# Optimization experiments

Hardware: AMD Instinct MI355X
Metric: run time of the kernel (lower is better)

The kernel has to match this reference:

```python
import jax, jax.numpy as jnp
import numpy as np

EPS = 1e-5
DIM_HEAD = 64
HEADS = 8

def layernorm(x, gamma, beta):
    mu = jnp.mean(x, axis=-1, keepdims=True)
    var = jnp.var(x, axis=-1, keepdims=True)
    return (x - mu) * jax.lax.rsqrt(var + EPS) * gamma + beta

def setup_inputs() -> dict:
    key = jax.random.key(0)
    ks = jax.random.split(key, 8)
    b, n, dh = 1, 896, 3072       # batch, enformer seq len, enformer_hidden_dim
    c, j, dc = 64, 127, 1024      # num contexts (tracks), context len, context_dim
    inner = HEADS * DIM_HEAD      # 512
    return {
        "embeddings": jax.random.normal(ks[0], (b, n, dh), jnp.float32),
        "context": jax.random.normal(ks[1], (c, j, dc), jnp.float32),
        "context_mask": jax.random.randint(ks[2], (b, j), 0, 2) > 0,
        "q_gamma": jnp.ones((dh,), jnp.float32),
        "q_beta": jnp.zeros((dh,), jnp.float32),
        "kv_gamma": jnp.ones((dc,), jnp.float32),
        "kv_beta": jnp.zeros((dc,), jnp.float32),
        "Wq": jax.random.normal(ks[3], (dh, inner), jnp.float32) * 0.02,
        "Wkv": jax.random.normal(ks[4], (dc, 2 * inner), jnp.float32) * 0.02,
        "null_k": jax.random.normal(ks[5], (inner,), jnp.float32),
        "null_v": jax.random.normal(ks[6], (inner,), jnp.float32),
        "Wo": jax.random.normal(ks[7], (inner, dh), jnp.float32) * 0.02,
        "bo": jnp.zeros((dh,), jnp.float32),
        "Wp": jax.random.normal(jax.random.fold_in(key, 9), (dh, 1), jnp.float32) * 0.02,
        "bp": jnp.zeros((1,), jnp.float32),
    }

def reference(embeddings, context, context_mask, q_gamma, q_beta, kv_gamma, kv_beta,
              Wq, Wkv, null_k, null_v, Wo, bo, Wp, bp):
    h, d = HEADS, DIM_HEAD
    scale = d ** -0.5
    b, n, dh = embeddings.shape
    c = context.shape[0]
    # projections
    q = layernorm(embeddings, q_gamma, q_beta) @ Wq            # (b, n, h*d)
    kv = layernorm(context, kv_gamma, kv_beta) @ Wkv           # (c, j, 2*h*d)
    k, v = jnp.split(kv, 2, axis=-1)
    # prepend null key/value token
    k = jnp.concatenate([jnp.broadcast_to(null_k, (c, 1, h * d)), k], axis=1)
    v = jnp.concatenate([jnp.broadcast_to(null_v, (c, 1, h * d)), v], axis=1)
    # split heads: (b, h, i, d) / (c, h, j, d)
    q = q.reshape(b, n, h, d).transpose(0, 2, 1, 3)
    k = k.reshape(c, -1, h, d).transpose(0, 2, 1, 3)
    v = v.reshape(c, -1, h, d).transpose(0, 2, 1, 3)
    sim = jnp.einsum('bhid,chjd->bchij', q, k) * scale         # (b, c, h, i, j+1)
    # mask: pad with True for the null token, broadcast over c, h, i
    mask = jnp.pad(context_mask, ((0, 0), (1, 0)), constant_values=True)
    sim = jnp.where(mask[:, None, None, None, :], sim, -jnp.finfo(sim.dtype).max)
    attn = jax.nn.softmax(sim, axis=-1)
    out = jnp.einsum('bchij,chjd->bchid', attn, v)             # (b, c, h, i, d)
    out = out.transpose(0, 1, 3, 2, 4).reshape(b, c, n, h * d)  # (b, c, n, h*d)
    branch = out @ Wo + bo                                     # (b, c, n, dh)
    emb = embeddings[:, None] + branch                         # (b, c, n, dh)
    pred = jax.nn.softplus((emb @ Wp + bp)[..., 0])            # (b, c, n)
    return pred.transpose(0, 2, 1)                             # (b, n, c)
```

## Files before the change

kernel.cpp:

```cpp
#include <hip/hip_runtime.h>
#include <math.h>

#define N_SEQ   896
#define DH      3072
#define NCTX    64
#define JLEN    127
#define DC      1024
#define HEADS   8
#define DHEAD   64
#define INNER   512
#define MKV     8128
#define MKVPAD  8192

typedef __bf16 bf16x8 __attribute__((ext_vector_type(8)));
typedef float  f32x4  __attribute__((ext_vector_type(4)));

#define OFF_EDOT   0LL
#define OFF_QBF    (OFF_EDOT + N_SEQ)
#define OFF_KBF    (OFF_QBF  + (long long)N_SEQ*INNER/2)
#define OFF_VPM    (OFF_KBF  + (long long)NCTX*128*INNER/2)
#define OFF_VPNULL (OFF_VPM  + (long long)MKV*8)
#define OFF_WOP    (OFF_VPNULL + 8)
#define OFF_BOP    (OFF_WOP  + INNER)
#define OFF_SBUF   (OFF_BOP  + 16)
#define OFF_ANQ    (OFF_SBUF + (long long)NCTX*HEADS*N_SEQ)
#define OFF_ANKV   (OFF_ANQ  + (long long)N_SEQ*DH/2)
#define OFF_WQT    (OFF_ANKV + (long long)MKVPAD*DC/2)
#define OFF_WKT    (OFF_WQT  + (long long)INNER*DH/2)
#define OFF_WVPT   (OFF_WKT  + (long long)INNER*DC/2)
#define OFF_QSL    (OFF_WVPT + 16*1024/2)

__device__ __forceinline__ void async_copy16(const __bf16* g, __bf16* l) {
    __builtin_amdgcn_global_load_lds(
        (const __attribute__((address_space(1))) unsigned int*)g,
        (__attribute__((address_space(3))) unsigned int*)l,
        16, 0, 0);
}

template <int P>
__device__ __forceinline__
void ln_row(const float* __restrict__ x,
            const float* __restrict__ gamma, const float* __restrict__ beta,
            const float* __restrict__ wp,
            __bf16* __restrict__ o, float* __restrict__ dotout) {
    const int K = P * 1024;
    float4 xv[P];
    float s = 0.f, ss = 0.f, dp = 0.f;
    #pragma unroll
    for (int p = 0; p < P; ++p) {
        xv[p] = *(const float4*)&x[p * 1024 + threadIdx.x * 4];
        s  += xv[p].x + xv[p].y + xv[p].z + xv[p].w;
        ss += xv[p].x * xv[p].x + xv[p].y * xv[p].y
            + xv[p].z * xv[p].z + xv[p].w * xv[p].w;
        if (wp) {
            float4 w4 = *(const float4*)&wp[p * 1024 + threadIdx.x * 4];
            dp += xv[p].x * w4.x + xv[p].y * w4.y + xv[p].z * w4.z + xv[p].w * w4.w;
        }
    }
    #pragma unroll
    for (int ofs = 32; ofs > 0; ofs >>= 1) {
        s  += __shfl_down(s,  ofs);
        ss += __shfl_down(ss, ofs);
        dp += __shfl_down(dp, ofs);
    }
    __shared__ float red[3][4];
    __shared__ float sh_mu, sh_rstd;
    int lane = threadIdx.x & 63, w = threadIdx.x >> 6;
    if (lane == 0) { red[0][w] = s; red[1][w] = ss; red[2][w] = dp; }
    __syncthreads();
    if (threadIdx.x == 0) {
        float S  = red[0][0] + red[0][1] + red[0][2] + red[0][3];
        float SS = red[1][0] + red[1][1] + red[1][2] + red[1][3];
        float m = S / K;
        sh_mu = m;
        sh_rstd = rsqrtf(SS / K - m * m + 1e-5f);
        if (dotout) *dotout = red[2][0] + red[2][1] + red[2][2] + red[2][3];
    }
    __syncthreads();
    float m = sh_mu, r = sh_rstd;
    #pragma unroll
    for (int p = 0; p < P; ++p) {
        int col = p * 1024 + threadIdx.x * 4;
        float4 g4 = *(const float4*)&gamma[col];
        float4 b4 = *(const float4*)&beta[col];
        __bf16 ov[4];
        ov[0] = (__bf16)((xv[p].x - m) * r * g4.x + b4.x);
        ov[1] = (__bf16)((xv[p].y - m) * r * g4.y + b4.y);
        ov[2] = (__bf16)((xv[p].z - m) * r * g4.z + b4.z);
        ov[3] = (__bf16)((xv[p].w - m) * r * g4.w + b4.w);
        *(ushort4*)&o[col] = *(ushort4*)ov;
    }
}

__global__ __launch_bounds__(256)
void ln_wop_kernel(const float* __restrict__ emb, const float* __restrict__ ctx,
                   const float* __restrict__ qg, const float* __restrict__ qb,
                   const float* __restrict__ kvg, const float* __restrict__ kvb,
                   const float* __restrict__ Wp, const float* __restrict__ Wo,
                   const float* __restrict__ bo,
                   __bf16* __restrict__ anq, __bf16* __restrict__ ankv,
                   float* __restrict__ edot, float* __restrict__ wop,
                   float* __restrict__ bop) {
    int b = blockIdx.x;
    if (b < N_SEQ) {
        ln_row<3>(emb + (long long)b * DH, qg, qb, Wp,
                  anq + (long long)b * DH, edot + b);
    } else if (b < N_SEQ + MKV) {
        int r = b - N_SEQ;
        ln_row<1>(ctx + (long long)r * DC, kvg, kvb, nullptr,
                  ankv + (long long)r * DC, nullptr);
    } else {
        int r = b - (N_SEQ + MKV);
        const float* src = (r < INNER) ? (Wo + (long long)r * DH) : bo;
        float s = 0.f;
        for (int k = threadIdx.x; k < DH; k += 256) s += src[k] * Wp[k];
        #pragma unroll
        for (int o = 32; o > 0; o >>= 1) s += __shfl_down(s, o);
        __shared__ float red2[4];
        int lane = threadIdx.x & 63, w = threadIdx.x >> 6;
        if (lane == 0) red2[w] = s;
        __syncthreads();
        if (threadIdx.x == 0) {
            float S = red2[0] + red2[1] + red2[2] + red2[3];
            if (r < INNER) wop[r] = S; else *bop = S;
        }
    }
}

__device__ __forceinline__
void transpose_tile(const float* __restrict__ src, int srcStride,
                    __bf16* __restrict__ dst, int dstStride,
                    int rb, int cb, float t[32][33]) {
    int tx = threadIdx.x & 31, ty = threadIdx.x >> 5;
    #pragma unroll
    for (int i = 0; i < 32; i += 8)
        t[ty + i][tx] = src[(long long)(rb + ty + i) * srcStride + cb + tx];
    __syncthreads();
    #pragma unroll
    for (int i = 0; i < 32; i += 8)
        dst[(long long)(cb + ty + i) * dstStride + rb + tx] = (__bf16)t[tx][ty + i];
}

__global__ __launch_bounds__(256)
void prep2_kernel(const float* __restrict__ Wq, const float* __restrict__ Wkv,
                  const float* __restrict__ wop,
                  const float* __restrict__ null_v, const float* __restrict__ null_k,
                  __bf16* __restrict__ wqt, __bf16* __restrict__ wkt,
                  __bf16* __restrict__ wvpt, float* __restrict__ vpnull,
                  __bf16* __restrict__ k_bf) {
    __shared__ float t[32][33];
    int b = blockIdx.x;
    if (b < 1536) {
        int rb = (b >> 4) * 32, cb = (b & 15) * 32;
        transpose_tile(Wq, INNER, wqt, DH, rb, cb, t);
    } else if (b < 2048) {
        int bi = b - 1536;
        int rb = (bi >> 4) * 32, cb = (bi & 15) * 32;
        transpose_tile(Wkv, 2 * INNER, wkt, DC, rb, cb, t);
    } else if (b < 2080) {
        int tt = (b - 2048) * 256 + threadIdx.x;
        int k = tt >> 3, h = tt & 7;
        const float* src = Wkv + (long long)k * (2 * INNER) + INNER + h * 64;
        const float* wv  = wop + h * 64;
        float s = 0.f;
        #pragma unroll 16
        for (int d = 0; d < 64; ++d) s += src[d] * wv[d];
        wvpt[h * 1024 + k] = (__bf16)s;
    } else {
        for (int i = threadIdx.x; i < 8 * 1024; i += 256)
            wvpt[8 * 1024 + i] = (__bf16)0.f;
        for (int i = threadIdx.x; i < NCTX * INNER; i += 256) {
            int c = i >> 9, d = i & 511;
            k_bf[(long long)(c * 128) * INNER + d] = (__bf16)null_k[d];
        }
        if (threadIdx.x < 8) {
            int h = threadIdx.x;
            float s = 0.f;
            #pragma unroll 16
            for (int d = 0; d < 64; ++d) s += null_v[h * 64 + d] * wop[h * 64 + d];
            vpnull[h] = s;
        }
    }
}

__global__ __launch_bounds__(256)
void proj_kernel(const __bf16* __restrict__ ANQ, const __bf16* __restrict__ WQT,
                 const __bf16* __restrict__ ANKV, const __bf16* __restrict__ WKT,
                 const __bf16* __restrict__ WVPT,
                 float* __restrict__ qsl, __bf16* __restrict__ kout,
                 float* __restrict__ vpm) {
    __shared__ __align__(16) __bf16 As[128 * 32];
    __shared__ __align__(16) __bf16 Bs[128 * 32];
    int b = blockIdx.x;
    int tid = threadIdx.x;
    int lane = tid & 63, w = tid >> 6;
    int n16 = lane & 15, quad = lane >> 4;
    int wr = (w >> 1) * 64, wc = (w & 1) * 64;

    const __bf16 *A, *B;
    int K, kbeg, kend, mode, slice = 0;
    long long m0, n0;
    if (b < 224) {
        mode = 0; slice = b / 28;
        int rem = b % 28;
        m0 = (long long)(rem % 7) * 128;
        n0 = (long long)(rem / 7) * 128;
        K = DH; kbeg = slice * 384; kend = kbeg + 384;
        A = ANQ; B = WQT;
    } else {
        mode = 1;
        int b2 = b - 224;
        m0 = (long long)(b2 & 63) * 128;
        n0 = (long long)(b2 >> 6) * 128;
        K = DC; kbeg = 0; kend = DC;
        A = ANKV; B = WKT;
    }
    bool dovp = (mode == 1) && (n0 == 0);

    const __bf16* aG = A + (m0 + (tid >> 2)) * K + (tid & 3) * 8;
    const __bf16* bG = B + (n0 + (tid >> 2)) * K + (tid & 3) * 8;
    __bf16* aL = As + tid * 8;
    __bf16* bL = Bs + tid * 8;

    f32x4 acc[4][4], accv[4];
    const f32x4 z = {0.f, 0.f, 0.f, 0.f};
    #pragma unroll
    for (int i = 0; i < 4; ++i) {
        accv[i] = z;
        #pragma unroll
        for (int j = 0; j < 4; ++j) acc[i][j] = z;
    }

    for (int k0 = kbeg; k0 < kend; k0 += 32) {
        async_copy16(aG + k0, aL);
        async_copy16(aG + (long long)64 * K + k0, aL + 2048);
        async_copy16(bG + k0, bL);
        async_copy16(bG + (long long)64 * K + k0, bL + 2048);
        bf16x8 bv;
        if (dovp) bv = *(const bf16x8*)&WVPT[n16 * 1024 + k0 + quad * 8];
        __syncthreads();
        bf16x8 af[4], bfr[4];
        #pragma unroll
        for (int i = 0; i < 4; ++i)
            af[i]  = *(const bf16x8*)&As[(wr + i * 16 + n16) * 32 + quad * 8];
        #pragma unroll
        for (int j = 0; j < 4; ++j)
            bfr[j] = *(const bf16x8*)&Bs[(wc + j * 16 + n16) * 32 + quad * 8];
        #pragma unroll
        for (int i = 0; i < 4; ++i)
            #pragma unroll
            for (int j = 0; j < 4; ++j)
                acc[i][j] = __builtin_amdgcn_mfma_f32_16x16x32_bf16(af[i], bfr[j], acc[i][j], 0, 0, 0);
        if (dovp) {
            #pragma unroll
            for (int i = 0; i < 4; ++i)
                accv[i] = __builtin_amdgcn_mfma_f32_16x16x32_bf16(af[i], bv, accv[i], 0, 0, 0);
        }
        __syncthreads();
    }

    if (mode == 0) {
        float* qdst = qsl + (long long)slice * (N_SEQ * INNER);
        #pragma unroll
        for (int i = 0; i < 4; ++i)
            #pragma unroll
            for (int r = 0; r < 4; ++r) {
                long long gr = m0 + wr + i * 16 + quad * 4 + r;
                #pragma unroll
                for (int j = 0; j < 4; ++j) {
                    long long gc = n0 + wc + j * 16 + n16;
                    qdst[gr * INNER + gc] = acc[i][j][r];
                }
            }
    } else {
        #pragma unroll
        for (int i = 0; i < 4; ++i)
            #pragma unroll
            for (int r = 0; r < 4; ++r) {
                long long gr = m0 + wr + i * 16 + quad * 4 + r;
                if (gr >= MKV) continue;
                int cc = (int)(gr / JLEN), jj = (int)(gr % JLEN);
                #pragma unroll
                for (int j = 0; j < 4; ++j) {
                    long long gc = n0 + wc + j * 16 + n16;
                    kout[((long long)(cc * 128) + jj + 1) * INNER + gc] = (__bf16)acc[i][j][r];
                }
                if (dovp && n16 < 8) vpm[gr * 8 + n16] = accv[i][r];
            }
    }
}

__global__ void qreduce_kernel(const float* __restrict__ qsl, __bf16* __restrict__ qbf) {
    int t = blockIdx.x * 256 + threadIdx.x;
    float s = 0.f;
    #pragma unroll
    for (int k = 0; k < 8; ++k) s += qsl[(long long)k * (N_SEQ * INNER) + t];
    qbf[t] = (__bf16)s;
}

#define KROW 72

__global__ __launch_bounds__(256)
void attn_mfma_kernel(const __bf16* __restrict__ qb, const __bf16* __restrict__ kb,
                      const float* __restrict__ vpm, const float* __restrict__ vpnull,
                      const int* __restrict__ mask, float* __restrict__ s_buf) {
    __shared__ __align__(16) __bf16 ksh[128 * KROW];
    __shared__ float vpsh[128];
    __shared__ float amsh[128];
    int ch = blockIdx.y;
    int h = ch & 7, c = ch >> 3;
    int tid = threadIdx.x;
    int lane = tid & 63, w = tid >> 6;
    int n16 = lane & 15, quad = lane >> 4;

    const __bf16* kbase = kb + (long long)(c * 128) * INNER + h * DHEAD;
    #pragma unroll
    for (int p = 0; p < 4; ++p) {
        int chunk = tid + p * 256;
        int row = chunk >> 3, o = chunk & 7;
        bf16x8 v = *(const bf16x8*)(kbase + (long long)row * INNER + o * 8);
        *(bf16x8*)&ksh[row * KROW + o * 8] = v;
    }
    if (tid < 128) {
        vpsh[tid] = (tid == 0) ? vpnull[h] : vpm[(long long)(c * JLEN + tid - 1) * 8 + h];
        amsh[tid] = (tid == 0) ? 0.f : (mask[tid - 1] ? 0.f : -3.0e38f);
    }
    __syncthreads();

    bf16x8 bF[8][2];
    #pragma unroll
    for (int t = 0; t < 8; ++t)
        #pragma unroll
        for (int s = 0; s < 2; ++s)
            bF[t][s] = *(const bf16x8*)&ksh[(t * 16 + n16) * KROW + s * 32 + quad * 8];

    float vpv[8], am[8];
    #pragma unroll
    for (int t = 0; t < 8; ++t) {
        vpv[t] = vpsh[t * 16 + n16];
        am[t]  = amsh[t * 16 + n16];
    }

    const __bf16* qbase = qb + h * DHEAD;
    bf16x8 aF[2][2];
    int r0s[2];
    #pragma unroll
    for (int it2 = 0; it2 < 2; ++it2) {
        int tile = blockIdx.x * 8 + it2 * 4 + w;
        r0s[it2] = tile * 16;
        const __bf16* qrow = qbase + (long long)(r0s[it2] + n16) * INNER + quad * 8;
        aF[it2][0] = *(const bf16x8*)(qrow);
        aF[it2][1] = *(const bf16x8*)(qrow + 32);
    }

    const f32x4 zero = {0.f, 0.f, 0.f, 0.f};
    #pragma unroll
    for (int it2 = 0; it2 < 2; ++it2) {
        int r0 = r0s[it2];
        f32x4 acc[8];
        #pragma unroll
        for (int t = 0; t < 8; ++t) {
            acc[t] = __builtin_amdgcn_mfma_f32_16x16x32_bf16(aF[it2][0], bF[t][0], zero,   0, 0, 0);
            acc[t] = __builtin_amdgcn_mfma_f32_16x16x32_bf16(aF[it2][1], bF[t][1], acc[t], 0, 0, 0);
        }
        float mloc = -3.0e38f;
        #pragma unroll
        for (int t = 0; t < 8; ++t)
            #pragma unroll
            for (int r = 0; r < 4; ++r)
                mloc = fmaxf(mloc, acc[t][r] * 0.125f + am[t]);
        #pragma unroll
        for (int o = 1; o < 16; o <<= 1) mloc = fmaxf(mloc, __shfl_xor(mloc, o, 16));
        float lr[4] = {0.f, 0.f, 0.f, 0.f}, pr[4] = {0.f, 0.f, 0.f, 0.f};
        #pragma unroll
        for (int t = 0; t < 8; ++t) {
            #pragma unroll
            for (int r = 0; r < 4; ++r) {
                float e = __expf(acc[t][r] * 0.125f + am[t] - mloc);
                lr[r] += e; pr[r] += e * vpv[t];
            }
        }
        #pragma unroll
        for (int o = 1; o < 16; o <<= 1) {
            #pragma unroll
            for (int r = 0; r < 4; ++r) {
                lr[r] += __shfl_xor(lr[r], o, 16);
                pr[r] += __shfl_xor(pr[r], o, 16);
            }
        }
        if (n16 == 0) {
            #pragma unroll
            for (int r = 0; r < 4; ++r)
                s_buf[(long long)ch * N_SEQ + r0 + quad * 4 + r] = pr[r] / lr[r];
        }
    }
}

__global__ void final_kernel(const float* __restrict__ s_buf,
                             const float* __restrict__ e_dot,
                             const float* __restrict__ bop,
                             const float* __restrict__ bp,
                             float* __restrict__ out) {
    int t = blockIdx.x * blockDim.x + threadIdx.x;
    if (t >= N_SEQ * NCTX) return;
    int n = t >> 6, c = t & 63;
    float s = 0.f;
    #pragma unroll
    for (int h = 0; h < HEADS; ++h) s += s_buf[((long long)(c * HEADS + h)) * N_SEQ + n];
    float x = e_dot[n] + s + *bop + *bp;
    out[t] = fmaxf(x, 0.f) + log1pf(__expf(-fabsf(x)));
}

extern "C" void kernel_launch(void* const* d_in, const int* in_sizes, int n_in,
                              void* d_out, int out_size, void* d_ws, size_t ws_size,
                              hipStream_t stream) {
    const float* emb   = (const float*)d_in[0];
    const float* ctx   = (const float*)d_in[1];
    const int*   cmask = (const int*)  d_in[2];
    const float* qg    = (const float*)d_in[3];
    const float* qb_   = (const float*)d_in[4];
    const float* kvg   = (const float*)d_in[5];
    const float* kvb   = (const float*)d_in[6];
    const float* Wq    = (const float*)d_in[7];
    const float* Wkv   = (const float*)d_in[8];
    const float* nullk = (const float*)d_in[9];
    const float* nullv = (const float*)d_in[10];
    const float* Wo    = (const float*)d_in[11];
    const float* bo    = (const float*)d_in[12];
    const float* Wp    = (const float*)d_in[13];
    const float* bp    = (const float*)d_in[14];
    float* out  = (float*)d_out;
    float* ws_f = (float*)d_ws;

    float*  EDOT   = ws_f + OFF_EDOT;
    __bf16* QBF    = (__bf16*)(ws_f + OFF_QBF);
    __bf16* KBF    = (__bf16*)(ws_f + OFF_KBF);
    float*  VPM    = ws_f + OFF_VPM;
    float*  VPNULL = ws_f + OFF_VPNULL;
    float*  WOP    = ws_f + OFF_WOP;
    float*  BOP    = ws_f + OFF_BOP;
    float*  SBUF   = ws_f + OFF_SBUF;
    __bf16* ANQ    = (__bf16*)(ws_f + OFF_ANQ);
    __bf16* ANKV   = (__bf16*)(ws_f + OFF_ANKV);
    __bf16* WQT    = (__bf16*)(ws_f + OFF_WQT);
    __bf16* WKT    = (__bf16*)(ws_f + OFF_WKT);
    __bf16* WVPT   = (__bf16*)(ws_f + OFF_WVPT);
    float*  QSL    = ws_f + OFF_QSL;

    ln_wop_kernel<<<N_SEQ + MKV + INNER + 1, 256, 0, stream>>>(
        emb, ctx, qg, qb_, kvg, kvb, Wp, Wo, bo, ANQ, ANKV, EDOT, WOP, BOP);
    prep2_kernel<<<2081, 256, 0, stream>>>(
        Wq, Wkv, WOP, nullv, nullk, WQT, WKT, WVPT, VPNULL, KBF);
    proj_kernel<<<480, 256, 0, stream>>>(ANQ, WQT, ANKV, WKT, WVPT, QSL, KBF, VPM);
    qreduce_kernel<<<(N_SEQ * INNER) / 256, 256, 0, stream>>>(QSL, QBF);
    attn_mfma_kernel<<<dim3(7, NCTX * HEADS), 256, 0, stream>>>(
        QBF, KBF, VPM, VPNULL, cmask, SBUF);
    final_kernel<<<(N_SEQ * NCTX + 255) / 256, 256, 0, stream>>>(SBUF, EDOT, BOP, bp, out);
}
```

Baseline: 216.6 us.

## Fuse prep into LN kernel, split-K KV projection, in-kernel last-block reduction

Moves the weight transposes and null-K init into the layernorm kernel and keeps a small kernel for the Wv·Wop products, which depend on the Wop result. The KV projection GEMM is now split over K into two slices, raising the grid from 480 to 736 blocks. The separate q-reduce kernel is replaced by atomic counters: the last block to finish each tile sums the split-K partials and writes the bf16 Q/K outputs. This removes a launch and improves occupancy, at the cost of writing and re-reading fp32 partials for K and adding atomics and fences.

```diff
diff --git a/kernel.cpp b/kernel.cpp
--- a/kernel.cpp
+++ b/kernel.cpp
@@ -29,6 +29,12 @@
 #define OFF_WKT    (OFF_WQT  + (long long)INNER*DH/2)
 #define OFF_WVPT   (OFF_WKT  + (long long)INNER*DC/2)
 #define OFF_QSL    (OFF_WVPT + 16*1024/2)
+#define OFF_KSL    (OFF_QSL  + 8LL*N_SEQ*INNER)
+#define OFF_VPSL   (OFF_KSL  + 2LL*MKVPAD*INNER)
+#define OFF_CNT    (OFF_VPSL + 2LL*MKVPAD*8)
+
+#define NQCNT 28
+#define NKCNT 256
 
 __device__ __forceinline__ void async_copy16(const __bf16* g, __bf16* l) {
     __builtin_amdgcn_global_load_lds(
@@ -92,25 +98,50 @@
     }
 }
 
+__device__ __forceinline__
+void transpose_tile(const float* __restrict__ src, int srcStride,
+                    __bf16* __restrict__ dst, int dstStride,
+                    int rb, int cb, float t[32][33]) {
+    int tx = threadIdx.x & 31, ty = threadIdx.x >> 5;
+    #pragma unroll
+    for (int i = 0; i < 32; i += 8)
+        t[ty + i][tx] = src[(long long)(rb + ty + i) * srcStride + cb + tx];
+    __syncthreads();
+    #pragma unroll
+    for (int i = 0; i < 32; i += 8)
+        dst[(long long)(cb + ty + i) * dstStride + rb + tx] = (__bf16)t[tx][ty + i];
+}
+
+#define B_LNQ   N_SEQ
+#define B_LNKV  (B_LNQ + MKV)
+#define B_WOPE  (B_LNKV + INNER + 1)
+#define B_TQ    (B_WOPE + 1536)
+#define B_TK    (B_TQ + 512)
+#define B_ALL   (B_TK + 1)
+
 __global__ __launch_bounds__(256)
-void ln_wop_kernel(const float* __restrict__ emb, const float* __restrict__ ctx,
-                   const float* __restrict__ qg, const float* __restrict__ qb,
-                   const float* __restrict__ kvg, const float* __restrict__ kvb,
-                   const float* __restrict__ Wp, const float* __restrict__ Wo,
-                   const float* __restrict__ bo,
-                   __bf16* __restrict__ anq, __bf16* __restrict__ ankv,
-                   float* __restrict__ edot, float* __restrict__ wop,
-                   float* __restrict__ bop) {
+void k1_kernel(const float* __restrict__ emb, const float* __restrict__ ctx,
+               const float* __restrict__ qg, const float* __restrict__ qb,
+               const float* __restrict__ kvg, const float* __restrict__ kvb,
+               const float* __restrict__ Wp, const float* __restrict__ Wo,
+               const float* __restrict__ bo, const float* __restrict__ Wq,
+               const float* __restrict__ Wkv, const float* __restrict__ null_k,
+               __bf16* __restrict__ anq, __bf16* __restrict__ ankv,
+               float* __restrict__ edot, float* __restrict__ wop,
+               float* __restrict__ bop, __bf16* __restrict__ wqt,
+               __bf16* __restrict__ wkt, __bf16* __restrict__ wvpt,
+               __bf16* __restrict__ k_bf, int* __restrict__ cnt) {
+    __shared__ float t[32][33];
     int b = blockIdx.x;
-    if (b < N_SEQ) {
+    if (b < B_LNQ) {
         ln_row<3>(emb + (long long)b * DH, qg, qb, Wp,
                   anq + (long long)b * DH, edot + b);
-    } else if (b < N_SEQ + MKV) {
-        int r = b - N_SEQ;
+    } else if (b < B_LNKV) {
+        int r = b - B_LNQ;
         ln_row<1>(ctx + (long long)r * DC, kvg, kvb, nullptr,
                   ankv + (long long)r * DC, nullptr);
-    } else {
-        int r = b - (N_SEQ + MKV);
+    } else if (b < B_WOPE) {
+        int r = b - B_LNKV;
         const float* src = (r < INNER) ? (Wo + (long long)r * DH) : bo;
         float s = 0.f;
         for (int k = threadIdx.x; k < DH; k += 256) s += src[k] * Wp[k];
@@ -124,41 +155,30 @@
             float S = red2[0] + red2[1] + red2[2] + red2[3];
             if (r < INNER) wop[r] = S; else *bop = S;
         }
-    }
-}
-
-__device__ __forceinline__
-void transpose_tile(const float* __restrict__ src, int srcStride,
-                    __bf16* __restrict__ dst, int dstStride,
-                    int rb, int cb, float t[32][33]) {
-    int tx = threadIdx.x & 31, ty = threadIdx.x >> 5;
-    #pragma unroll
-    for (int i = 0; i < 32; i += 8)
-        t[ty + i][tx] = src[(long long)(rb + ty + i) * srcStride + cb + tx];
-    __syncthreads();
-    #pragma unroll
-    for (int i = 0; i < 32; i += 8)
-        dst[(long long)(cb + ty + i) * dstStride + rb + tx] = (__bf16)t[tx][ty + i];
+    } else if (b < B_TQ) {
+        int bi = b - B_WOPE;
+        transpose_tile(Wq, INNER, wqt, DH, (bi >> 4) * 32, (bi & 15) * 32, t);
+    } else if (b < B_TK) {
+        int bi = b - B_TQ;
+        transpose_tile(Wkv, 2 * INNER, wkt, DC, (bi >> 4) * 32, (bi & 15) * 32, t);
+    } else {
+        for (int i = threadIdx.x; i < 8 * 1024; i += 256)
+            wvpt[8 * 1024 + i] = (__bf16)0.f;
+        for (int i = threadIdx.x; i < NCTX * INNER; i += 256) {
+            int c = i >> 9, d = i & 511;
+            k_bf[(long long)(c * 128) * INNER + d] = (__bf16)null_k[d];
+        }
+        if (threadIdx.x < NQCNT + NKCNT) cnt[threadIdx.x] = 0;
+    }
 }
 
 __global__ __launch_bounds__(256)
-void prep2_kernel(const float* __restrict__ Wq, const float* __restrict__ Wkv,
-                  const float* __restrict__ wop,
-                  const float* __restrict__ null_v, const float* __restrict__ null_k,
-                  __bf16* __restrict__ wqt, __bf16* __restrict__ wkt,
-                  __bf16* __restrict__ wvpt, float* __restrict__ vpnull,
-                  __bf16* __restrict__ k_bf) {
-    __shared__ float t[32][33];
+void k1b_kernel(const float* __restrict__ Wkv, const float* __restrict__ wop,
+                const float* __restrict__ null_v,
+                __bf16* __restrict__ wvpt, float* __restrict__ vpnull) {
     int b = blockIdx.x;
-    if (b < 1536) {
-        int rb = (b >> 4) * 32, cb = (b & 15) * 32;
-        transpose_tile(Wq, INNER, wqt, DH, rb, cb, t);
-    } else if (b < 2048) {
-        int bi = b - 1536;
-        int rb = (bi >> 4) * 32, cb = (bi & 15) * 32;
-        transpose_tile(Wkv, 2 * INNER, wkt, DC, rb, cb, t);
-    } else if (b < 2080) {
-        int tt = (b - 2048) * 256 + threadIdx.x;
+    if (b < 32) {
+        int tt = b * 256 + threadIdx.x;
         int k = tt >> 3, h = tt & 7;
         const float* src = Wkv + (long long)k * (2 * INNER) + INNER + h * 64;
         const float* wv  = wop + h * 64;
@@ -166,20 +186,12 @@
         #pragma unroll 16
         for (int d = 0; d < 64; ++d) s += src[d] * wv[d];
         wvpt[h * 1024 + k] = (__bf16)s;
-    } else {
-        for (int i = threadIdx.x; i < 8 * 1024; i += 256)
-            wvpt[8 * 1024 + i] = (__bf16)0.f;
-        for (int i = threadIdx.x; i < NCTX * INNER; i += 256) {
-            int c = i >> 9, d = i & 511;
-            k_bf[(long long)(c * 128) * INNER + d] = (__bf16)null_k[d];
-        }
-        if (threadIdx.x < 8) {
-            int h = threadIdx.x;
-            float s = 0.f;
-            #pragma unroll 16
-            for (int d = 0; d < 64; ++d) s += null_v[h * 64 + d] * wop[h * 64 + d];
-            vpnull[h] = s;
-        }
+    } else if (threadIdx.x < 8) {
+        int h = threadIdx.x;
+        float s = 0.f;
+        #pragma unroll 16
+        for (int d = 0; d < 64; ++d) s += null_v[h * 64 + d] * wop[h * 64 + d];
+        vpnull[h] = s;
     }
 }
 
@@ -187,10 +199,11 @@
 void proj_kernel(const __bf16* __restrict__ ANQ, const __bf16* __restrict__ WQT,
                  const __bf16* __restrict__ ANKV, const __bf16* __restrict__ WKT,
                  const __bf16* __restrict__ WVPT,
-                 float* __restrict__ qsl, __bf16* __restrict__ kout,
-                 float* __restrict__ vpm) {
+                 float* qsl, float* ksl, float* vpsl,
+                 __bf16* qbf, __bf16* kbf, float* vpm, int* cnt) {
     __shared__ __align__(16) __bf16 As[128 * 32];
     __shared__ __align__(16) __bf16 Bs[128 * 32];
+    __shared__ int sh_last;
     int b = blockIdx.x;
     int tid = threadIdx.x;
     int lane = tid & 63, w = tid >> 6;
@@ -198,21 +211,21 @@
     int wr = (w >> 1) * 64, wc = (w & 1) * 64;
 
     const __bf16 *A, *B;
-    int K, kbeg, kend, mode, slice = 0;
+    int K, kbeg, kend, mode, slice, tile;
     long long m0, n0;
     if (b < 224) {
-        mode = 0; slice = b / 28;
-        int rem = b % 28;
-        m0 = (long long)(rem % 7) * 128;
-        n0 = (long long)(rem / 7) * 128;
+        mode = 0; slice = b / 28; tile = b % 28;
+        m0 = (long long)(tile % 7) * 128;
+        n0 = (long long)(tile / 7) * 128;
         K = DH; kbeg = slice * 384; kend = kbeg + 384;
         A = ANQ; B = WQT;
     } else {
         mode = 1;
         int b2 = b - 224;
-        m0 = (long long)(b2 & 63) * 128;
-        n0 = (long long)(b2 >> 6) * 128;
-        K = DC; kbeg = 0; kend = DC;
+        slice = b2 >> 8; tile = b2 & 255;
+        m0 = (long long)(tile & 63) * 128;
+        n0 = (long long)(tile >> 6) * 128;
+        K = DC; kbeg = slice * 512; kend = kbeg + 512;
         A = ANKV; B = WKT;
     }
     bool dovp = (mode == 1) && (n0 == 0);
@@ -260,42 +273,83 @@
     }
 
     if (mode == 0) {
-        float* qdst = qsl + (long long)slice * (N_SEQ * INNER);
+        float* dst = qsl + (long long)slice * (N_SEQ * INNER);
         #pragma unroll
         for (int i = 0; i < 4; ++i)
             #pragma unroll
             for (int r = 0; r < 4; ++r) {
                 long long gr = m0 + wr + i * 16 + quad * 4 + r;
                 #pragma unroll
-                for (int j = 0; j < 4; ++j) {
-                    long long gc = n0 + wc + j * 16 + n16;
-                    qdst[gr * INNER + gc] = acc[i][j][r];
-                }
+                for (int j = 0; j < 4; ++j)
+                    dst[gr * INNER + n0 + wc + j * 16 + n16] = acc[i][j][r];
             }
     } else {
+        float* dst = ksl + (long long)slice * ((long long)MKVPAD * INNER);
         #pragma unroll
         for (int i = 0; i < 4; ++i)
             #pragma unroll
             for (int r = 0; r < 4; ++r) {
                 long long gr = m0 + wr + i * 16 + quad * 4 + r;
-                if (gr >= MKV) continue;
-                int cc = (int)(gr / JLEN), jj = (int)(gr % JLEN);
                 #pragma unroll
-                for (int j = 0; j < 4; ++j) {
-                    long long gc = n0 + wc + j * 16 + n16;
-                    kout[((long long)(cc * 128) + jj + 1) * INNER + gc] = (__bf16)acc[i][j][r];
-                }
-                if (dovp && n16 < 8) vpm[gr * 8 + n16] = accv[i][r];
+                for (int j = 0; j < 4; ++j)
+                    dst[gr * INNER + n0 + wc + j * 16 + n16] = acc[i][j][r];
+                if (dovp && n16 < 8)
+                    vpsl[(long long)slice * (MKVPAD * 8) + gr * 8 + n16] = accv[i][r];
             }
     }
-}
-
-__global__ void qreduce_kernel(const float* __restrict__ qsl, __bf16* __restrict__ qbf) {
-    int t = blockIdx.x * 256 + threadIdx.x;
-    float s = 0.f;
-    #pragma unroll
-    for (int k = 0; k < 8; ++k) s += qsl[(long long)k * (N_SEQ * INNER) + t];
-    qbf[t] = (__bf16)s;
+
+    __threadfence();
+    __syncthreads();
+    if (tid == 0) {
+        int old = atomicAdd(&cnt[(mode == 0) ? tile : (NQCNT + tile)], 1);
+        sh_last = (old == ((mode == 0) ? 7 : 1));
+    }
+    __syncthreads();
+    if (!sh_last) return;
+    __threadfence();
+
+    if (mode == 0) {
+        #pragma unroll
+        for (int k = 0; k < 16; ++k) {
+            int cid = tid + k * 256;
+            int row = cid >> 5, c4 = (cid & 31) * 4;
+            long long row_g = m0 + row, col_g = n0 + c4;
+            float4 s = {0.f, 0.f, 0.f, 0.f};
+            #pragma unroll
+            for (int sl = 0; sl < 8; ++sl) {
+                float4 v = *(const float4*)&qsl[(long long)sl * (N_SEQ * INNER) + row_g * INNER + col_g];
+                s.x += v.x; s.y += v.y; s.z += v.z; s.w += v.w;
+            }
+            __bf16 ov[4] = {(__bf16)s.x, (__bf16)s.y, (__bf16)s.z, (__bf16)s.w};
+            *(ushort4*)&qbf[row_g * INNER + col_g] = *(ushort4*)ov;
+        }
+    } else {
+        const float* s0 = ksl;
+        const float* s1 = ksl + (long long)MKVPAD * INNER;
+        #pragma unroll
+        for (int k = 0; k < 16; ++k) {
+            int cid = tid + k * 256;
+            int row = cid >> 5, c4 = (cid & 31) * 4;
+            long long row_g = m0 + row;
+            if (row_g >= MKV) continue;
+            long long col_g = n0 + c4;
+            int cc = (int)(row_g / JLEN), jj = (int)(row_g % JLEN);
+            float4 a = *(const float4*)&s0[row_g * INNER + col_g];
+            float4 bb = *(const float4*)&s1[row_g * INNER + col_g];
+            __bf16 ov[4] = {(__bf16)(a.x + bb.x), (__bf16)(a.y + bb.y),
+                            (__bf16)(a.z + bb.z), (__bf16)(a.w + bb.w)};
+            *(ushort4*)&kbf[((long long)(cc * 128) + jj + 1) * INNER + col_g] = *(ushort4*)ov;
+        }
+        if (n0 == 0) {
+            for (int idx = tid; idx < 1024; idx += 256) {
+                int row = idx >> 3, hh = idx & 7;
+                long long row_g = m0 + row;
+                if (row_g >= MKV) continue;
+                vpm[row_g * 8 + hh] = vpsl[row_g * 8 + hh]
+                                    + vpsl[(long long)MKVPAD * 8 + row_g * 8 + hh];
+            }
+        }
+    }
 }
 
 #define KROW 72
@@ -446,13 +500,16 @@
     __bf16* WKT    = (__bf16*)(ws_f + OFF_WKT);
     __bf16* WVPT   = (__bf16*)(ws_f + OFF_WVPT);
     float*  QSL    = ws_f + OFF_QSL;
-
-    ln_wop_kernel<<<N_SEQ + MKV + INNER + 1, 256, 0, stream>>>(
-        emb, ctx, qg, qb_, kvg, kvb, Wp, Wo, bo, ANQ, ANKV, EDOT, WOP, BOP);
-    prep2_kernel<<<2081, 256, 0, stream>>>(
-        Wq, Wkv, WOP, nullv, nullk, WQT, WKT, WVPT, VPNULL, KBF);
-    proj_kernel<<<480, 256, 0, stream>>>(ANQ, WQT, ANKV, WKT, WVPT, QSL, KBF, VPM);
-    qreduce_kernel<<<(N_SEQ * INNER) / 256, 256, 0, stream>>>(QSL, QBF);
+    float*  KSL    = ws_f + OFF_KSL;
+    float*  VPSL   = ws_f + OFF_VPSL;
+    int*    CNT    = (int*)(ws_f + OFF_CNT);
+
+    k1_kernel<<<B_ALL, 256, 0, stream>>>(
+        emb, ctx, qg, qb_, kvg, kvb, Wp, Wo, bo, Wq, Wkv, nullk,
+        ANQ, ANKV, EDOT, WOP, BOP, WQT, WKT, WVPT, KBF, CNT);
+    k1b_kernel<<<33, 256, 0, stream>>>(Wkv, WOP, nullv, WVPT, VPNULL);
+    proj_kernel<<<736, 256, 0, stream>>>(
+        ANQ, WQT, ANKV, WKT, WVPT, QSL, KSL, VPSL, QBF, KBF, VPM, CNT);
     attn_mfma_kernel<<<dim3(7, NCTX * HEADS), 256, 0, stream>>>(
         QBF, KBF, VPM, VPNULL, cmask, SBUF);
     final_kernel<<<(N_SEQ * NCTX + 255) / 256, 256, 0, stream>>>(SBUF, EDOT, BOP, bp, out);
```

Measured after the change: 384.6 us. +77.6%, slower.

## Merge layernorm and weight-prep kernels, retile KV projection, vectorize q reduction

Applied to the files above, without the earlier changes.

The layernorm, Wo·Wp fold, weight transposes and null-token setup now run in one kernel, removing a launch and a dependency boundary. The Wo·Wp fold is computed per head inside the blocks that build the folded V weights, so the separate wop buffer goes away. The KV projection moves from 128x128 to 128x64 tiles, raising the block count (736 vs 480) for better CU occupancy. The q split-K reduction now works on float4 values. The costs are some redundant Wo·Wp work and a lower MFMA-to-load ratio in the smaller KV tiles.

```diff
diff --git a/kernel.cpp b/kernel.cpp
--- a/kernel.cpp
+++ b/kernel.cpp
@@ -20,8 +20,7 @@
 #define OFF_KBF    (OFF_QBF  + (long long)N_SEQ*INNER/2)
 #define OFF_VPM    (OFF_KBF  + (long long)NCTX*128*INNER/2)
 #define OFF_VPNULL (OFF_VPM  + (long long)MKV*8)
-#define OFF_WOP    (OFF_VPNULL + 8)
-#define OFF_BOP    (OFF_WOP  + INNER)
+#define OFF_BOP    (OFF_VPNULL + 8)
 #define OFF_SBUF   (OFF_BOP  + 16)
 #define OFF_ANQ    (OFF_SBUF + (long long)NCTX*HEADS*N_SEQ)
 #define OFF_ANKV   (OFF_ANQ  + (long long)N_SEQ*DH/2)
@@ -92,41 +91,6 @@
     }
 }
 
-__global__ __launch_bounds__(256)
-void ln_wop_kernel(const float* __restrict__ emb, const float* __restrict__ ctx,
-                   const float* __restrict__ qg, const float* __restrict__ qb,
-                   const float* __restrict__ kvg, const float* __restrict__ kvb,
-                   const float* __restrict__ Wp, const float* __restrict__ Wo,
-                   const float* __restrict__ bo,
-                   __bf16* __restrict__ anq, __bf16* __restrict__ ankv,
-                   float* __restrict__ edot, float* __restrict__ wop,
-                   float* __restrict__ bop) {
-    int b = blockIdx.x;
-    if (b < N_SEQ) {
-        ln_row<3>(emb + (long long)b * DH, qg, qb, Wp,
-                  anq + (long long)b * DH, edot + b);
-    } else if (b < N_SEQ + MKV) {
-        int r = b - N_SEQ;
-        ln_row<1>(ctx + (long long)r * DC, kvg, kvb, nullptr,
-                  ankv + (long long)r * DC, nullptr);
-    } else {
-        int r = b - (N_SEQ + MKV);
-        const float* src = (r < INNER) ? (Wo + (long long)r * DH) : bo;
-        float s = 0.f;
-        for (int k = threadIdx.x; k < DH; k += 256) s += src[k] * Wp[k];
-        #pragma unroll
-        for (int o = 32; o > 0; o >>= 1) s += __shfl_down(s, o);
-        __shared__ float red2[4];
-        int lane = threadIdx.x & 63, w = threadIdx.x >> 6;
-        if (lane == 0) red2[w] = s;
-        __syncthreads();
-        if (threadIdx.x == 0) {
-            float S = red2[0] + red2[1] + red2[2] + red2[3];
-            if (r < INNER) wop[r] = S; else *bop = S;
-        }
-    }
-}
-
 __device__ __forceinline__
 void transpose_tile(const float* __restrict__ src, int srcStride,
                     __bf16* __restrict__ dst, int dstStride,
@@ -141,44 +105,88 @@
         dst[(long long)(cb + ty + i) * dstStride + rb + tx] = (__bf16)t[tx][ty + i];
 }
 
+#define B_LNQ   N_SEQ
+#define B_LNKV  (B_LNQ + MKV)
+#define B_TQ    (B_LNKV + 1536)
+#define B_TK    (B_TQ + 512)
+#define B_WVP   (B_TK + 8)
+#define B_BOP   (B_WVP + 1)
+#define B_ALL   (B_BOP + 1)
+
 __global__ __launch_bounds__(256)
-void prep2_kernel(const float* __restrict__ Wq, const float* __restrict__ Wkv,
-                  const float* __restrict__ wop,
-                  const float* __restrict__ null_v, const float* __restrict__ null_k,
-                  __bf16* __restrict__ wqt, __bf16* __restrict__ wkt,
-                  __bf16* __restrict__ wvpt, float* __restrict__ vpnull,
-                  __bf16* __restrict__ k_bf) {
+void k1_kernel(const float* __restrict__ emb, const float* __restrict__ ctx,
+               const float* __restrict__ qg, const float* __restrict__ qb,
+               const float* __restrict__ kvg, const float* __restrict__ kvb,
+               const float* __restrict__ Wp, const float* __restrict__ Wo,
+               const float* __restrict__ bo, const float* __restrict__ Wq,
+               const float* __restrict__ Wkv, const float* __restrict__ null_k,
+               const float* __restrict__ null_v,
+               __bf16* __restrict__ anq, __bf16* __restrict__ ankv,
+               float* __restrict__ edot, float* __restrict__ bop,
+               __bf16* __restrict__ wqt, __bf16* __restrict__ wkt,
+               __bf16* __restrict__ wvpt, float* __restrict__ vpnull,
+               __bf16* __restrict__ k_bf) {
     __shared__ float t[32][33];
     int b = blockIdx.x;
-    if (b < 1536) {
-        int rb = (b >> 4) * 32, cb = (b & 15) * 32;
-        transpose_tile(Wq, INNER, wqt, DH, rb, cb, t);
-    } else if (b < 2048) {
-        int bi = b - 1536;
-        int rb = (bi >> 4) * 32, cb = (bi & 15) * 32;
-        transpose_tile(Wkv, 2 * INNER, wkt, DC, rb, cb, t);
-    } else if (b < 2080) {
-        int tt = (b - 2048) * 256 + threadIdx.x;
-        int k = tt >> 3, h = tt & 7;
-        const float* src = Wkv + (long long)k * (2 * INNER) + INNER + h * 64;
-        const float* wv  = wop + h * 64;
+    int tid = threadIdx.x;
+    if (b < B_LNQ) {
+        ln_row<3>(emb + (long long)b * DH, qg, qb, Wp,
+                  anq + (long long)b * DH, edot + b);
+    } else if (b < B_LNKV) {
+        int r = b - B_LNQ;
+        ln_row<1>(ctx + (long long)r * DC, kvg, kvb, nullptr,
+                  ankv + (long long)r * DC, nullptr);
+    } else if (b < B_TQ) {
+        int bi = b - B_LNKV;
+        transpose_tile(Wq, INNER, wqt, DH, (bi >> 4) * 32, (bi & 15) * 32, t);
+    } else if (b < B_TK) {
+        int bi = b - B_TQ;
+        transpose_tile(Wkv, 2 * INNER, wkt, DC, (bi >> 4) * 32, (bi & 15) * 32, t);
+    } else if (b < B_WVP) {
+        int h = b - B_TK;
+        __shared__ float part[64][4];
+        __shared__ float wops[64];
+        int v = tid >> 2, p = tid & 3;
+        const float* row = Wo + ((long long)(h * 64 + v)) * DH + p * 768;
+        const float* wpp = Wp + p * 768;
         float s = 0.f;
-        #pragma unroll 16
-        for (int d = 0; d < 64; ++d) s += src[d] * wv[d];
-        wvpt[h * 1024 + k] = (__bf16)s;
+        #pragma unroll 8
+        for (int e = 0; e < 768; ++e) s += row[e] * wpp[e];
+        part[v][p] = s;
+        __syncthreads();
+        if (tid < 64) wops[tid] = part[tid][0] + part[tid][1] + part[tid][2] + part[tid][3];
+        __syncthreads();
+        if (tid == 64) {
+            float sn = 0.f;
+            #pragma unroll 16
+            for (int d = 0; d < 64; ++d) sn += null_v[h * 64 + d] * wops[d];
+            vpnull[h] = sn;
+        }
+        #pragma unroll
+        for (int kk = 0; kk < 4; ++kk) {
+            int k = kk * 256 + tid;
+            const float* src = Wkv + (long long)k * (2 * INNER) + INNER + h * 64;
+            float sv = 0.f;
+            #pragma unroll 16
+            for (int d = 0; d < 64; ++d) sv += src[d] * wops[d];
+            wvpt[h * 1024 + k] = (__bf16)sv;
+        }
+    } else if (b < B_BOP) {
+        float s = 0.f;
+        for (int k = tid; k < DH; k += 256) s += bo[k] * Wp[k];
+        #pragma unroll
+        for (int o = 32; o > 0; o >>= 1) s += __shfl_down(s, o);
+        __shared__ float red2[4];
+        int lane = tid & 63, w = tid >> 6;
+        if (lane == 0) red2[w] = s;
+        __syncthreads();
+        if (tid == 0) *bop = red2[0] + red2[1] + red2[2] + red2[3];
     } else {
-        for (int i = threadIdx.x; i < 8 * 1024; i += 256)
+        for (int i = tid; i < 8 * 1024; i += 256)
             wvpt[8 * 1024 + i] = (__bf16)0.f;
-        for (int i = threadIdx.x; i < NCTX * INNER; i += 256) {
+        for (int i = tid; i < NCTX * INNER; i += 256) {
             int c = i >> 9, d = i & 511;
             k_bf[(long long)(c * 128) * INNER + d] = (__bf16)null_k[d];
-        }
-        if (threadIdx.x < 8) {
-            int h = threadIdx.x;
-            float s = 0.f;
-            #pragma unroll 16
-            for (int d = 0; d < 64; ++d) s += null_v[h * 64 + d] * wop[h * 64 + d];
-            vpnull[h] = s;
         }
     }
 }
@@ -195,84 +203,95 @@
     int tid = threadIdx.x;
     int lane = tid & 63, w = tid >> 6;
     int n16 = lane & 15, quad = lane >> 4;
-    int wr = (w >> 1) * 64, wc = (w & 1) * 64;
-
-    const __bf16 *A, *B;
-    int K, kbeg, kend, mode, slice = 0;
-    long long m0, n0;
+    const f32x4 z = {0.f, 0.f, 0.f, 0.f};
+
     if (b < 224) {
-        mode = 0; slice = b / 28;
-        int rem = b % 28;
-        m0 = (long long)(rem % 7) * 128;
-        n0 = (long long)(rem / 7) * 128;
-        K = DH; kbeg = slice * 384; kend = kbeg + 384;
-        A = ANQ; B = WQT;
-    } else {
-        mode = 1;
-        int b2 = b - 224;
-        m0 = (long long)(b2 & 63) * 128;
-        n0 = (long long)(b2 >> 6) * 128;
-        K = DC; kbeg = 0; kend = DC;
-        A = ANKV; B = WKT;
-    }
-    bool dovp = (mode == 1) && (n0 == 0);
-
-    const __bf16* aG = A + (m0 + (tid >> 2)) * K + (tid & 3) * 8;
-    const __bf16* bG = B + (n0 + (tid >> 2)) * K + (tid & 3) * 8;
-    __bf16* aL = As + tid * 8;
-    __bf16* bL = Bs + tid * 8;
-
-    f32x4 acc[4][4], accv[4];
-    const f32x4 z = {0.f, 0.f, 0.f, 0.f};
-    #pragma unroll
-    for (int i = 0; i < 4; ++i) {
-        accv[i] = z;
-        #pragma unroll
-        for (int j = 0; j < 4; ++j) acc[i][j] = z;
-    }
-
-    for (int k0 = kbeg; k0 < kend; k0 += 32) {
-        async_copy16(aG + k0, aL);
-        async_copy16(aG + (long long)64 * K + k0, aL + 2048);
-        async_copy16(bG + k0, bL);
-        async_copy16(bG + (long long)64 * K + k0, bL + 2048);
-        bf16x8 bv;
-        if (dovp) bv = *(const bf16x8*)&WVPT[n16 * 1024 + k0 + quad * 8];
-        __syncthreads();
-        bf16x8 af[4], bfr[4];
+        int slice = b / 28, tile = b % 28;
+        long long m0 = (long long)(tile % 7) * 128;
+        long long n0 = (long long)(tile / 7) * 128;
+        int kbeg = slice * 384, kend = kbeg + 384;
+        int wr = (w >> 1) * 64, wc = (w & 1) * 64;
+        const __bf16* aG = ANQ + (m0 + (tid >> 2)) * DH + (tid & 3) * 8;
+        const __bf16* bG = WQT + (n0 + (tid >> 2)) * DH + (tid & 3) * 8;
+        __bf16* aL = As + tid * 8;
+        __bf16* bL = Bs + tid * 8;
+        f32x4 acc[4][4];
         #pragma unroll
         for (int i = 0; i < 4; ++i)
-            af[i]  = *(const bf16x8*)&As[(wr + i * 16 + n16) * 32 + quad * 8];
-        #pragma unroll
-        for (int j = 0; j < 4; ++j)
-            bfr[j] = *(const bf16x8*)&Bs[(wc + j * 16 + n16) * 32 + quad * 8];
-        #pragma unroll
-        for (int i = 0; i < 4; ++i)
+            #pragma unroll
+            for (int j = 0; j < 4; ++j) acc[i][j] = z;
+        for (int k0 = kbeg; k0 < kend; k0 += 32) {
+            async_copy16(aG + k0, aL);
+            async_copy16(aG + (long long)64 * DH + k0, aL + 2048);
+            async_copy16(bG + k0, bL);
+            async_copy16(bG + (long long)64 * DH + k0, bL + 2048);
+            __syncthreads();
+            bf16x8 af[4], bfr[4];
+            #pragma unroll
+            for (int i = 0; i < 4; ++i)
+                af[i]  = *(const bf16x8*)&As[(wr + i * 16 + n16) * 32 + quad * 8];
             #pragma unroll
             for (int j = 0; j < 4; ++j)
-                acc[i][j] = __builtin_amdgcn_mfma_f32_16x16x32_bf16(af[i], bfr[j], acc[i][j], 0, 0, 0);
-        if (dovp) {
+                bfr[j] = *(const bf16x8*)&Bs[(wc + j * 16 + n16) * 32 + quad * 8];
             #pragma unroll
             for (int i = 0; i < 4; ++i)
-                accv[i] = __builtin_amdgcn_mfma_f32_16x16x32_bf16(af[i], bv, accv[i], 0, 0, 0);
-        }
-        __syncthreads();
-    }
-
-    if (mode == 0) {
-        float* qdst = qsl + (long long)slice * (N_SEQ * INNER);
+                #pragma unroll
+                for (int j = 0; j < 4; ++j)
+                    acc[i][j] = __builtin_amdgcn_mfma_f32_16x16x32_bf16(af[i], bfr[j], acc[i][j], 0, 0, 0);
+            __syncthreads();
+        }
+        float* dst = qsl + (long long)slice * (N_SEQ * INNER);
         #pragma unroll
         for (int i = 0; i < 4; ++i)
             #pragma unroll
             for (int r = 0; r < 4; ++r) {
                 long long gr = m0 + wr + i * 16 + quad * 4 + r;
                 #pragma unroll
-                for (int j = 0; j < 4; ++j) {
-                    long long gc = n0 + wc + j * 16 + n16;
-                    qdst[gr * INNER + gc] = acc[i][j][r];
-                }
+                for (int j = 0; j < 4; ++j)
+                    dst[gr * INNER + n0 + wc + j * 16 + n16] = acc[i][j][r];
             }
     } else {
+        int b2 = b - 224;
+        long long m0 = (long long)(b2 >> 3) * 128;
+        long long n0 = (long long)(b2 & 7) * 64;
+        int wr = (w >> 1) * 64, wc = (w & 1) * 32;
+        bool dovp = (n0 == 0) && ((w & 1) == 0);
+        const __bf16* aG = ANKV + (m0 + (tid >> 2)) * DC + (tid & 3) * 8;
+        const __bf16* bG = WKT  + (n0 + (tid >> 2)) * DC + (tid & 3) * 8;
+        __bf16* aL = As + tid * 8;
+        __bf16* bL = Bs + tid * 8;
+        f32x4 acc[4][2], accv[4];
+        #pragma unroll
+        for (int i = 0; i < 4; ++i) {
+            accv[i] = z;
+            acc[i][0] = z; acc[i][1] = z;
+        }
+        for (int k0 = 0; k0 < DC; k0 += 32) {
+            async_copy16(aG + k0, aL);
+            async_copy16(aG + (long long)64 * DC + k0, aL + 2048);
+            async_copy16(bG + k0, bL);
+            bf16x8 bv;
+            if (dovp) bv = *(const bf16x8*)&WVPT[n16 * 1024 + k0 + quad * 8];
+            __syncthreads();
+            bf16x8 af[4], bfr[2];
+            #pragma unroll
+            for (int i = 0; i < 4; ++i)
+                af[i]  = *(const bf16x8*)&As[(wr + i * 16 + n16) * 32 + quad * 8];
+            #pragma unroll
+            for (int j = 0; j < 2; ++j)
+                bfr[j] = *(const bf16x8*)&Bs[(wc + j * 16 + n16) * 32 + quad * 8];
+            #pragma unroll
+            for (int i = 0; i < 4; ++i) {
+                acc[i][0] = __builtin_amdgcn_mfma_f32_16x16x32_bf16(af[i], bfr[0], acc[i][0], 0, 0, 0);
+                acc[i][1] = __builtin_amdgcn_mfma_f32_16x16x32_bf16(af[i], bfr[1], acc[i][1], 0, 0, 0);
+            }
+            if (dovp) {
+                #pragma unroll
+                for (int i = 0; i < 4; ++i)
+                    accv[i] = __builtin_amdgcn_mfma_f32_16x16x32_bf16(af[i], bv, accv[i], 0, 0, 0);
+            }
+            __syncthreads();
+        }
         #pragma unroll
         for (int i = 0; i < 4; ++i)
             #pragma unroll
@@ -281,7 +300,7 @@
                 if (gr >= MKV) continue;
                 int cc = (int)(gr / JLEN), jj = (int)(gr % JLEN);
                 #pragma unroll
-                for (int j = 0; j < 4; ++j) {
+                for (int j = 0; j < 2; ++j) {
                     long long gc = n0 + wc + j * 16 + n16;
                     kout[((long long)(cc * 128) + jj + 1) * INNER + gc] = (__bf16)acc[i][j][r];
                 }
@@ -291,11 +310,16 @@
 }
 
 __global__ void qreduce_kernel(const float* __restrict__ qsl, __bf16* __restrict__ qbf) {
-    int t = blockIdx.x * 256 + threadIdx.x;
-    float s = 0.f;
-    #pragma unroll
-    for (int k = 0; k < 8; ++k) s += qsl[(long long)k * (N_SEQ * INNER) + t];
-    qbf[t] = (__bf16)s;
+    int t4 = blockIdx.x * 256 + threadIdx.x;
+    const int SL = N_SEQ * INNER / 4;
+    float4 s = {0.f, 0.f, 0.f, 0.f};
+    #pragma unroll
+    for (int k = 0; k < 8; ++k) {
+        float4 v = ((const float4*)qsl)[(long long)k * SL + t4];
+        s.x += v.x; s.y += v.y; s.z += v.z; s.w += v.w;
+    }
+    __bf16 ov[4] = {(__bf16)s.x, (__bf16)s.y, (__bf16)s.z, (__bf16)s.w};
+    ((ushort4*)qbf)[t4] = *(ushort4*)ov;
 }
 
 #define KROW 72
@@ -437,7 +461,6 @@
     __bf16* KBF    = (__bf16*)(ws_f + OFF_KBF);
     float*  VPM    = ws_f + OFF_VPM;
     float*  VPNULL = ws_f + OFF_VPNULL;
-    float*  WOP    = ws_f + OFF_WOP;
     float*  BOP    = ws_f + OFF_BOP;
     float*  SBUF   = ws_f + OFF_SBUF;
     __bf16* ANQ    = (__bf16*)(ws_f + OFF_ANQ);
@@ -447,12 +470,12 @@
     __bf16* WVPT   = (__bf16*)(ws_f + OFF_WVPT);
     float*  QSL    = ws_f + OFF_QSL;
 
-    ln_wop_kernel<<<N_SEQ + MKV + INNER + 1, 256, 0, stream>>>(
-        emb, ctx, qg, qb_, kvg, kvb, Wp, Wo, bo, ANQ, ANKV, EDOT, WOP, BOP);
-    prep2_kernel<<<2081, 256, 0, stream>>>(
-        Wq, Wkv, WOP, nullv, nullk, WQT, WKT, WVPT, VPNULL, KBF);
-    proj_kernel<<<480, 256, 0, stream>>>(ANQ, WQT, ANKV, WKT, WVPT, QSL, KBF, VPM);
-    qreduce_kernel<<<(N_SEQ * INNER) / 256, 256, 0, stream>>>(QSL, QBF);
+    k1_kernel<<<B_ALL, 256, 0, stream>>>(
+        emb, ctx, qg, qb_, kvg, kvb, Wp, Wo, bo, Wq, Wkv, nullk, nullv,
+        ANQ, ANKV, EDOT, BOP, WQT, WKT, WVPT, VPNULL, KBF);
+    proj_kernel<<<736, 256, 0, stream>>>(
+        ANQ, WQT, ANKV, WKT, WVPT, QSL, KBF, VPM);
+    qreduce_kernel<<<(N_SEQ * INNER / 4) / 256, 256, 0, stream>>>(QSL, QBF);
     attn_mfma_kernel<<<dim3(7, NCTX * HEADS), 256, 0, stream>>>(
         QBF, KBF, VPM, VPNULL, cmask, SBUF);
     final_kernel<<<(N_SEQ * NCTX + 255) / 256, 256, 0, stream>>>(SBUF, EDOT, BOP, bp, out);
```

New measurement: 252.0 us. 16.4% more time.
